# Optimization experiments

Hardware: AMD Instinct MI355X
Metric: run time of the kernel (lower is better)

## Reference

```python
import jax, jax.numpy as jnp
import numpy as np
import math

B, L, HID = 2, 1024, 1536
NH, HD = 24, 64
DSSM = NH * HD            # 1536 (expand = 1)
QKV = 3 * DSSM
DCONV = 2
EPS = 1e-6


def _silu(u):
    return u * jax.nn.sigmoid(u)


def setup_inputs() -> dict:
    key = jax.random.key(0)
    ks = jax.random.split(key, 10)
    x = jax.random.normal(ks[0], (B, L, HID), dtype=jnp.float32)
    w_qkv = jax.random.normal(ks[1], (QKV, HID), dtype=jnp.float32) / math.sqrt(HID)
    conv_w = jax.random.normal(ks[2], (QKV, DCONV), dtype=jnp.float32) * 0.5  # depthwise causal conv, k=2
    w_dt = jax.random.normal(ks[3], (NH, HID), dtype=jnp.float32) * 0.02
    # dt_bias init exactly as in the torch module
    dt = jnp.exp(jax.random.uniform(ks[4], (NH,)) * (math.log(0.1) - math.log(0.001)) + math.log(0.001))
    dt = jnp.clip(dt, 1e-4, None)
    dt_bias = dt + jnp.log(-jnp.expm1(-dt))
    a_log = jnp.log(jax.random.uniform(ks[5], (NH,), minval=1.0, maxval=16.0))
    D = jnp.ones((NH, HD), dtype=jnp.float32)
    w_z = jax.random.normal(ks[6], (DSSM, HID), dtype=jnp.float32) / math.sqrt(HID)
    b_z = jnp.zeros((DSSM,), dtype=jnp.float32)
    rms_w = jnp.ones((DSSM,), dtype=jnp.float32)
    w_o = jax.random.normal(ks[7], (HID, DSSM), dtype=jnp.float32) / math.sqrt(DSSM)
    return dict(x=x, w_qkv=w_qkv, conv_w=conv_w, w_dt=w_dt, dt_bias=dt_bias,
                a_log=a_log, D=D, w_z=w_z, b_z=b_z, rms_w=rms_w, w_o=w_o)


def reference(x, w_qkv, conv_w, w_dt, dt_bias, a_log, D, w_z, b_z, rms_w, w_o):
    # qkv projection  [B,L,3*DSSM]
    qkv = jnp.einsum('blh,qh->blq', x, w_qkv)
    # depthwise causal conv1d (kernel size 2, padding k-1, trimmed to L)
    prev = jnp.pad(qkv, ((0, 0), (1, 0), (0, 0)))[:, :L]
    qkv = _silu(prev * conv_w[:, 0] + qkv * conv_w[:, 1])
    q, k, v = jnp.split(qkv, 3, axis=-1)
    q = q.reshape(B, L, NH, HD)
    k = k.reshape(B, L, NH, HD)
    v = v.reshape(B, L, NH, HD)
    # dt discretization: softplus(dt_proj(x) + dt_bias)   [B,L,NH]
    dt = jax.nn.softplus(jnp.einsum('blh,nh->bln', x, w_dt) + dt_bias)
    A = -jnp.exp(a_log)              # [NH], negative
    dA = dt * A                      # [B,L,NH]
    cs = jnp.transpose(jnp.cumsum(dA, axis=1), (0, 2, 1))   # [B,NH,L]
    diff = cs[:, :, :, None] - cs[:, :, None, :]            # [B,NH,L,L], <=0 on causal part
    causal = jnp.tril(jnp.ones((L, L), dtype=bool))
    decay = jnp.exp(jnp.where(causal, diff, -jnp.inf))      # segment-sum decay matrix
    # quadratic SSD (attention) form of the selective scan
    scores = jnp.einsum('bihd,bjhd->bhij', q, k) * decay
    scores = scores * jnp.transpose(dt, (0, 2, 1))[:, :, None, :]  # dt_j on keys (B-discretization)
    y = jnp.einsum('bhij,bjhd->bihd', scores, v)
    y = y + v * D                    # D skip connection
    y = y.reshape(B, L, DSSM)
    # z gate + RMSNorm + output projection
    z = jnp.einsum('blh,dh->bld', x, w_z) + b_z
    y = y * _silu(z)
    y = y * jax.lax.rsqrt(jnp.mean(y * y, axis=-1, keepdims=True) + EPS) * rms_w
    return jnp.einsum('bld,hd->blh', y, w_o)
```

## Files before the change

### kernel.cpp

```cpp
#include <hip/hip_runtime.h>
#include <hip/hip_bf16.h>
#include <math.h>

#define B_ 2
#define L_ 1024
#define HID_ 1536
#define NH_ 24
#define HD_ 64
#define DSSM_ 1536
#define QKV_ 4608
#define M_ 2048

typedef __attribute__((ext_vector_type(8))) short short8;
typedef __attribute__((ext_vector_type(4))) short short4e;
typedef __attribute__((ext_vector_type(4))) float floatx4;

__device__ __forceinline__ void gload_lds16(const short* g, short* l)
{
    __builtin_amdgcn_global_load_lds(
        (const __attribute__((address_space(1))) void*)g,
        (__attribute__((address_space(3))) void*)l,
        16, 0, 0);
}

__device__ __forceinline__ float bfs2f(short s)
{
    unsigned u = ((unsigned)(unsigned short)s) << 16;
    float f; __builtin_memcpy(&f, &u, 4); return f;
}
__device__ __forceinline__ short f2bfs(float f)
{
    __hip_bfloat16 h = __float2bfloat16(f);
    short s; __builtin_memcpy(&s, &h, 2); return s;
}

__device__ const int kIt[30] = {0,1,2,3,4,5, 6,6, 7,7, 8,8, 9,9, 10,10, 11,11,
                                12,12,12, 13,13,13, 14,14,14, 15,15,15};
__device__ const int kS[30]  = {0,0,0,0,0,0, 0,1, 0,1, 0,1, 0,1, 0,1, 0,1,
                                0,1,2, 0,1,2, 0,1,2, 0,1,2};

#define CN0 (M_ * HID_)
#define CN1 (QKV_ * HID_)
#define CN2 (DSSM_ * HID_)
#define CN3 (HID_ * DSSM_)
__global__ void cast_all_kernel(
    const float* __restrict__ x,  const float* __restrict__ wq,
    const float* __restrict__ wz, const float* __restrict__ wo,
    __hip_bfloat16* __restrict__ xb,
    __hip_bfloat16* __restrict__ wcat,
    __hip_bfloat16* __restrict__ wob)
{
    int i = (blockIdx.x * 256 + threadIdx.x) * 4;
    const float* src; __hip_bfloat16* dst; int off;
    if (i < CN0)                   { src = x;  dst = xb;         off = i; }
    else if (i < CN0 + CN1)        { src = wq; dst = wcat;       off = i - CN0; }
    else if (i < CN0 + CN1 + CN2)  { src = wz; dst = wcat + CN1; off = i - CN0 - CN1; }
    else                           { src = wo; dst = wob;        off = i - CN0 - CN1 - CN2; }
    float4 f = *reinterpret_cast<const float4*>(src + off);
    dst[off]     = __float2bfloat16(f.x);
    dst[off + 1] = __float2bfloat16(f.y);
    dst[off + 2] = __float2bfloat16(f.z);
    dst[off + 3] = __float2bfloat16(f.w);
}

#define MFMA_ __builtin_amdgcn_mfma_f32_16x16x32_bf16
#define BAR_() __builtin_amdgcn_s_barrier()
#define SCHED_ __builtin_amdgcn_sched_barrier(0)

#define CSTR 200

__global__ __launch_bounds__(256, 2) void gemm_qkvz_128(
    const __hip_bfloat16* __restrict__ A,
    const __hip_bfloat16* __restrict__ Bm,
    __hip_bfloat16* __restrict__ qkv_out,
    float* __restrict__ z_out,
    const float* __restrict__ b_z)
{
    extern __shared__ short lds[];
    const int K  = HID_;
    const int NT = K / 64;
    const int tid   = threadIdx.x;
    const int lane  = tid & 63;
    const int wave  = tid >> 6;
    const int col16 = lane & 15;
    const int quad  = lane >> 4;
    const int wm = wave >> 1;
    const int wn = wave & 1;
    const int rowblk = blockIdx.y * 128;
    const int colblk = blockIdx.x * 192;

    const short* Ap = reinterpret_cast<const short*>(A);
    const short* Bp = reinterpret_cast<const short*>(Bm);

    const int o  = tid * 16;
    const int s  = o ^ (((o >> 7) & 7) << 4);
    const int sr = s >> 7;
    const int sc = (s & 127) >> 1;

    const int mask = (col16 & 7) << 4;
    const int e0 = ((quad * 16)      ^ mask) >> 1;
    const int e1 = ((64 + quad * 16) ^ mask) >> 1;
    const int arow = (wm * 64 + col16) * 64;
    const int brow = (wn * 96 + col16) * 64;

    floatx4 acc[4][6] = {};

    auto STAGE_ALL = [&](int c, int t) {
        const short* ga = Ap + (size_t)(rowblk + sr) * K + t * 64 + sc;
        short* da = &lds[c * 8192 + tid * 8];
#pragma unroll
        for (int u = 0; u < 4; ++u)
            gload_lds16(ga + (size_t)(u * 32) * K, da + u * 2048);
        const short* gb = Bp + (size_t)(colblk + sr) * K + t * 64 + sc;
        short* db = &lds[16384 + c * 12288 + tid * 8];
#pragma unroll
        for (int u = 0; u < 6; ++u)
            gload_lds16(gb + (size_t)(u * 32) * K, db + u * 2048);
    };

    STAGE_ALL(0, 0);
    asm volatile("s_waitcnt vmcnt(0)" ::: "memory");
    SCHED_;
    BAR_();

    for (int t = 0; t < NT; ++t) {
        const int cur = t & 1;
        if (t + 1 < NT) STAGE_ALL(cur ^ 1, t + 1);

        const int Ab = cur * 8192;
        const int Bb = 16384 + cur * 12288;
        short8 af0[4], af1[4], bf0[6], bf1[6];
#pragma unroll
        for (int m = 0; m < 4; ++m) {
            af0[m] = *reinterpret_cast<const short8*>(&lds[Ab + arow + m * 1024 + e0]);
            af1[m] = *reinterpret_cast<const short8*>(&lds[Ab + arow + m * 1024 + e1]);
        }
#pragma unroll
        for (int n = 0; n < 6; ++n) {
            bf0[n] = *reinterpret_cast<const short8*>(&lds[Bb + brow + n * 1024 + e0]);
            bf1[n] = *reinterpret_cast<const short8*>(&lds[Bb + brow + n * 1024 + e1]);
        }
        asm volatile("s_waitcnt lgkmcnt(0)" ::: "memory");
        SCHED_;

        __builtin_amdgcn_s_setprio(1);
#pragma unroll
        for (int m = 0; m < 4; ++m)
#pragma unroll
            for (int n = 0; n < 6; ++n) {
                acc[m][n] = MFMA_(af0[m], bf0[n], acc[m][n], 0, 0, 0);
                acc[m][n] = MFMA_(af1[m], bf1[n], acc[m][n], 0, 0, 0);
            }
        __builtin_amdgcn_s_setprio(0);

        asm volatile("s_waitcnt vmcnt(0)" ::: "memory");
        SCHED_;
        BAR_();
    }

    if (blockIdx.x < 24) {
        const int rb = wm * 64 + quad * 4;
        const int cb = wn * 96 + col16;
#pragma unroll
        for (int m = 0; m < 4; ++m)
#pragma unroll
            for (int n = 0; n < 6; ++n)
#pragma unroll
                for (int r = 0; r < 4; ++r)
                    lds[(rb + m * 16 + r) * CSTR + cb + n * 16] =
                        f2bfs(acc[m][n][r]);
        __syncthreads();
        const int row = tid >> 1;
        const int seg = tid & 1;
        const short* srcp = &lds[row * CSTR + seg * 96];
        short* dstp = reinterpret_cast<short*>(qkv_out)
                    + (size_t)(rowblk + row) * QKV_ + colblk + seg * 96;
#pragma unroll
        for (int j = 0; j < 12; ++j)
            *reinterpret_cast<short8*>(dstp + j * 8) =
                *reinterpret_cast<const short8*>(srcp + j * 8);
    } else {
        const int row0  = rowblk + wm * 64;
        const int col0g = colblk + wn * 96 - QKV_;
#pragma unroll
        for (int m = 0; m < 4; ++m)
#pragma unroll
            for (int n = 0; n < 6; ++n)
#pragma unroll
                for (int r = 0; r < 4; ++r) {
                    int row = row0 + m * 16 + quad * 4 + r;
                    int col = col0g + n * 16 + col16;
                    z_out[(size_t)row * DSSM_ + col] = acc[m][n][r] + b_z[col];
                }
    }
}

template<int OUTMODE>
__global__ __launch_bounds__(256) void gemm_nt(
    const __hip_bfloat16* __restrict__ A,
    const __hip_bfloat16* __restrict__ Bm,
    void* __restrict__ Cv,
    const float* __restrict__ bias,
    int M, int N, int K)
{
    const int lane  = threadIdx.x & 63;
    const int wave  = threadIdx.x >> 6;
    const int col16 = lane & 15;
    const int quad  = lane >> 4;
    const int wr    = wave >> 1;
    const int wc    = wave & 1;
    const int rowblk = blockIdx.y * 128;
    const int colblk = blockIdx.x * 128;

    const short* Ap = reinterpret_cast<const short*>(A);
    const short* Bp = reinterpret_cast<const short*>(Bm);

    __shared__ alignas(16) short As[128 * 32];
    __shared__ alignas(16) short Bs[128 * 32];

    const int srow = lane >> 2;
    const int scol = (lane & 3) * 8;

    floatx4 acc[4][4] = {};

    for (int k0 = 0; k0 < K; k0 += 32) {
#pragma unroll
        for (int s2 = 0; s2 < 2; ++s2) {
            const int seg = wave * 2 + s2;
            gload_lds16(Ap + (size_t)(rowblk + seg * 16 + srow) * K + k0 + scol,
                        &As[seg * 512]);
            gload_lds16(Bp + (size_t)(colblk + seg * 16 + srow) * K + k0 + scol,
                        &Bs[seg * 512]);
        }
        __syncthreads();

        short8 af[4], bf[4];
#pragma unroll
        for (int t = 0; t < 4; ++t) {
            af[t] = *reinterpret_cast<const short8*>(
                &As[(wr * 64 + t * 16 + col16) * 32 + quad * 8]);
            bf[t] = *reinterpret_cast<const short8*>(
                &Bs[(wc * 64 + t * 16 + col16) * 32 + quad * 8]);
        }
#pragma unroll
        for (int mt = 0; mt < 4; ++mt)
#pragma unroll
            for (int nt = 0; nt < 4; ++nt)
                acc[mt][nt] = __builtin_amdgcn_mfma_f32_16x16x32_bf16(
                    af[mt], bf[nt], acc[mt][nt], 0, 0, 0);
        __syncthreads();
    }

    const int row0 = rowblk + wr * 64;
    const int col0 = colblk + wc * 64;
#pragma unroll
    for (int mt = 0; mt < 4; ++mt) {
#pragma unroll
        for (int nt = 0; nt < 4; ++nt) {
#pragma unroll
            for (int r = 0; r < 4; ++r) {
                int row = row0 + mt * 16 + quad * 4 + r;
                int col = col0 + nt * 16 + col16;
                float v = acc[mt][nt][r];
                if (OUTMODE == 1) v += bias[col];
                if (OUTMODE == 2)
                    ((__hip_bfloat16*)Cv)[(size_t)row * N + col] = __float2bfloat16(v);
                else
                    ((float*)Cv)[(size_t)row * N + col] = v;
            }
        }
    }
}

__global__ void conv_silu_kernel(
    const __hip_bfloat16* __restrict__ raw,
    const float* __restrict__ conv_w,
    __hip_bfloat16* __restrict__ q,
    __hip_bfloat16* __restrict__ k,
    __hip_bfloat16* __restrict__ v)
{
    int idx8 = blockIdx.x * 256 + threadIdx.x;
    int c8 = (idx8 % (QKV_ / 8)) * 8;
    int ml = idx8 / (QKV_ / 8);
    int l  = ml % L_;
    int b  = ml / L_;

    const short* base = reinterpret_cast<const short*>(raw) + (size_t)ml * QKV_ + c8;
    short8 curv = *reinterpret_cast<const short8*>(base);
    short8 prevv = {};
    if (l > 0) prevv = *reinterpret_cast<const short8*>(base - QKV_);

    float4 w0 = *reinterpret_cast<const float4*>(conv_w + c8 * 2);
    float4 w1 = *reinterpret_cast<const float4*>(conv_w + c8 * 2 + 4);
    float4 w2 = *reinterpret_cast<const float4*>(conv_w + c8 * 2 + 8);
    float4 w3 = *reinterpret_cast<const float4*>(conv_w + c8 * 2 + 12);
    const float wa[16] = {w0.x, w0.y, w0.z, w0.w, w1.x, w1.y, w1.z, w1.w,
                          w2.x, w2.y, w2.z, w2.w, w3.x, w3.y, w3.z, w3.w};

    short8 outv;
#pragma unroll
    for (int j = 0; j < 8; ++j) {
        float u = bfs2f(prevv[j]) * wa[2 * j] + bfs2f(curv[j]) * wa[2 * j + 1];
        u = fmaxf(u, -80.f);
        outv[j] = f2bfs(u / (1.f + __expf(-u)));
    }

    int part = c8 / DSSM_;
    int cc   = c8 % DSSM_;
    int nh   = cc >> 6;
    int d    = cc & 63;
    __hip_bfloat16* dst = (part == 0) ? q : ((part == 1) ? k : v);
    *reinterpret_cast<short8*>(
        reinterpret_cast<short*>(dst) + (((size_t)b * NH_ + nh) * L_ + l) * HD_ + d)
        = outv;
}

__global__ __launch_bounds__(256) void dtproj_kernel(
    const float* __restrict__ x,
    const float* __restrict__ w_dt,
    const float* __restrict__ dt_bias,
    const float* __restrict__ a_log,
    float* __restrict__ dt,
    float* __restrict__ dA)
{
    const int tid  = threadIdx.x;
    const int wave = tid >> 6;
    const int lane = tid & 63;
    const int m0   = blockIdx.x * 8 + wave * 2;

    float4 xa[2][6];
#pragma unroll
    for (int rr = 0; rr < 2; ++rr)
#pragma unroll
        for (int j = 0; j < 6; ++j)
            xa[rr][j] = *reinterpret_cast<const float4*>(
                x + (size_t)(m0 + rr) * HID_ + lane * 4 + j * 256);

    float acc0[NH_], acc1[NH_];
#pragma unroll
    for (int n = 0; n < NH_; ++n) {
        float s0 = 0.f, s1 = 0.f;
#pragma unroll
        for (int j = 0; j < 6; ++j) {
            float4 w = *reinterpret_cast<const float4*>(
                w_dt + (size_t)n * HID_ + lane * 4 + j * 256);
            s0 += xa[0][j].x * w.x + xa[0][j].y * w.y
                + xa[0][j].z * w.z + xa[0][j].w * w.w;
            s1 += xa[1][j].x * w.x + xa[1][j].y * w.y
                + xa[1][j].z * w.z + xa[1][j].w * w.w;
        }
        acc0[n] = s0;
        acc1[n] = s1;
    }

#pragma unroll
    for (int off = 32; off; off >>= 1) {
#pragma unroll
        for (int n = 0; n < NH_; ++n) {
            acc0[n] += __shfl_xor(acc0[n], off, 64);
            acc1[n] += __shfl_xor(acc1[n], off, 64);
        }
    }

    if (lane < NH_) {
        const int n = lane;
        float bias = dt_bias[n];
        float Aval = -__expf(a_log[n]);
        float v0 = acc0[n] + bias;
        float v1 = acc1[n] + bias;
        v0 = (v0 > 20.f) ? v0 : log1pf(__expf(v0));
        v1 = (v1 > 20.f) ? v1 : log1pf(__expf(v1));
        int b0 = m0 / L_, l0 = m0 % L_;
        size_t o0 = ((size_t)b0 * NH_ + n) * L_ + l0;
        dt[o0]     = v0;
        dA[o0]     = v0 * Aval;
        dt[o0 + 1] = v1;
        dA[o0 + 1] = v1 * Aval;
    }
}

__global__ void cumsum_kernel(const float* __restrict__ dA, float* __restrict__ cs)
{
    int bnh  = blockIdx.x;
    int lane = threadIdx.x;
    const float* src = dA + (size_t)bnh * L_;
    float* dst       = cs + (size_t)bnh * L_;

    float loc[16];
    float run = 0.f;
#pragma unroll
    for (int t = 0; t < 16; ++t) { run += src[lane * 16 + t]; loc[t] = run; }
    float tot = run;
    float sc = tot;
#pragma unroll
    for (int off = 1; off < 64; off <<= 1) {
        float o = __shfl_up(sc, off, 64);
        if (lane >= off) sc += o;
    }
    float offset = sc - tot;
#pragma unroll
    for (int t = 0; t < 16; ++t) dst[lane * 16 + t] = loc[t] + offset;
}

__global__ __launch_bounds__(256) void vdt_transpose_kernel(
    const __hip_bfloat16* __restrict__ v,
    const float* __restrict__ dt,
    __hip_bfloat16* __restrict__ vt)
{
    const int lt0 = blockIdx.x * 64;
    const int bnh = blockIdx.z * NH_ + blockIdx.y;
    const int tid = threadIdx.x;

    __shared__ short T[64][72];

    {
        int row = tid >> 2;
        int cc  = (tid & 3) * 16;
        const short* sp = reinterpret_cast<const short*>(v)
                        + ((size_t)bnh * L_ + lt0 + row) * HD_ + cc;
        float dtr = dt[(size_t)bnh * L_ + lt0 + row];
        short8 a = *reinterpret_cast<const short8*>(sp);
        short8 b = *reinterpret_cast<const short8*>(sp + 8);
#pragma unroll
        for (int j = 0; j < 8; ++j) {
            T[row][cc + j]     = f2bfs(bfs2f(a[j]) * dtr);
            T[row][cc + 8 + j] = f2bfs(bfs2f(b[j]) * dtr);
        }
    }
    __syncthreads();
    {
        int d  = tid >> 2;
        int lc = (tid & 3) * 16;
        short8 o0, o1;
#pragma unroll
        for (int j = 0; j < 8; ++j) {
            o0[j] = T[lc + j][d];
            o1[j] = T[lc + 8 + j][d];
        }
        short* dst = reinterpret_cast<short*>(vt)
                   + ((size_t)bnh * HD_ + d) * L_ + lt0 + lc;
        *reinterpret_cast<short8*>(dst)     = o0;
        *reinterpret_cast<short8*>(dst + 8) = o1;
    }
}

__global__ __launch_bounds__(256) void attn_kernel(
    const __hip_bfloat16* __restrict__ q,
    const __hip_bfloat16* __restrict__ k,
    const __hip_bfloat16* __restrict__ vt,
    const float* __restrict__ cs,
    float* __restrict__ p0,
    float* __restrict__ p1,
    float* __restrict__ p2)
{
    const int pidx = blockIdx.x;
    const int it   = kIt[pidx];
    const int sl   = kS[pidx];
    const int nh   = blockIdx.y;
    const int b    = blockIdx.z;
    const int tid  = threadIdx.x;
    const int lane = tid & 63;
    const int wave = tid >> 6;
    const int col  = lane & 15;
    const int quad = lane >> 4;
    const int bnh  = b * NH_ + nh;
    const int iw0  = it * 64 + wave * 16;

    float* pout = (sl == 0) ? p0 : ((sl == 1) ? p1 : p2);

    const short* qp  = reinterpret_cast<const short*>(q);
    const short* kp  = reinterpret_cast<const short*>(k);
    const short* vtp = reinterpret_cast<const short*>(vt);

    __shared__ alignas(16) short Ks[4096];
    __shared__ alignas(16) short Ps[4 * 16 * 72];
    __shared__ float Cj[384];

    const int jbase = sl * 384;
    const int jlim  = min(384, L_ - jbase);
    if (tid < (jlim >> 2))
        *reinterpret_cast<float4*>(&Cj[tid * 4]) =
            *reinterpret_cast<const float4*>(cs + (size_t)bnh * L_ + jbase + tid * 4);

    const short* qrow = qp + ((size_t)bnh * L_ + iw0 + col) * HD_;
    short8 aq0 = *reinterpret_cast<const short8*>(qrow + quad * 8);
    short8 aq1 = *reinterpret_cast<const short8*>(qrow + 32 + quad * 8);

    float csr[4];
#pragma unroll
    for (int r = 0; r < 4; ++r)
        csr[r] = cs[(size_t)bnh * L_ + iw0 + quad * 4 + r];

    auto STAGE_K = [&](int jt2) {
        const short* gk = kp + ((size_t)bnh * L_ + jt2 * 64 + wave * 16 + (lane >> 2)) * HD_
                        + (lane & 3) * 8;
        gload_lds16(gk,      &Ks[wave * 512 + lane * 8]);
        gload_lds16(gk + 32, &Ks[2048 + wave * 512 + lane * 8]);
    };

    const int jt_beg = sl * 6;
    const int jt_end = min(sl * 6 + 5, it);

    STAGE_K(jt_beg);

    floatx4 accO[4] = {};

    for (int jt = jt_beg; jt <= jt_end; ++jt) {
        const int j0 = jt * 64;

        asm volatile("s_waitcnt vmcnt(0)" ::: "memory");
        SCHED_;
        __syncthreads();

        short8 bv[2][4];
#pragma unroll
        for (int c = 0; c < 2; ++c) {
            if (j0 + c * 32 <= iw0 + 15) {
#pragma unroll
                for (int nt = 0; nt < 4; ++nt)
                    bv[c][nt] = *reinterpret_cast<const short8*>(
                        vtp + ((size_t)bnh * HD_ + nt * 16 + col) * L_
                            + j0 + c * 32 + quad * 8);
            }
        }

#pragma unroll
        for (int s = 0; s < 4; ++s) {
            int jsub = j0 + s * 16;
            if (jsub <= iw0 + 15) {
                short8 bk0 = *reinterpret_cast<const short8*>(
                    &Ks[(s * 16 + col) * 32 + quad * 8]);
                short8 bk1 = *reinterpret_cast<const short8*>(
                    &Ks[2048 + (s * 16 + col) * 32 + quad * 8]);
                floatx4 sc = {};
                sc = __builtin_amdgcn_mfma_f32_16x16x32_bf16(aq0, bk0, sc, 0, 0, 0);
                sc = __builtin_amdgcn_mfma_f32_16x16x32_bf16(aq1, bk1, sc, 0, 0, 0);
                int j = jsub + col;
                float csj = Cj[j - jbase];
#pragma unroll
                for (int r = 0; r < 4; ++r) {
                    int i = iw0 + quad * 4 + r;
                    float e = (j <= i) ? __expf(csr[r] - csj) : 0.f;
                    Ps[wave * 1152 + (quad * 4 + r) * 72 + s * 16 + col] =
                        f2bfs(sc[r] * e);
                }
            } else if (j0 + (s >> 1) * 32 <= iw0 + 15) {
#pragma unroll
                for (int r = 0; r < 4; ++r)
                    Ps[wave * 1152 + (quad * 4 + r) * 72 + s * 16 + col] = 0;
            }
        }

#pragma unroll
        for (int c = 0; c < 2; ++c) {
            if (j0 + c * 32 > iw0 + 15) continue;
            short8 pa = *reinterpret_cast<const short8*>(
                &Ps[wave * 1152 + col * 72 + c * 32 + quad * 8]);
#pragma unroll
            for (int nt = 0; nt < 4; ++nt)
                accO[nt] = __builtin_amdgcn_mfma_f32_16x16x32_bf16(
                    pa, bv[c][nt], accO[nt], 0, 0, 0);
        }

        __syncthreads();
        if (jt < jt_end) STAGE_K(jt + 1);
    }

#pragma unroll
    for (int nt = 0; nt < 4; ++nt) {
#pragma unroll
        for (int r = 0; r < 4; ++r) {
            int i  = iw0 + quad * 4 + r;
            int dv = nt * 16 + col;
            pout[((size_t)b * L_ + i) * DSSM_ + nh * HD_ + dv] = accO[nt][r];
        }
    }
}

__global__ __launch_bounds__(256) void gate_rms_kernel(
    const float* __restrict__ p0,
    const float* __restrict__ p1,
    const float* __restrict__ p2,
    const float* __restrict__ z,
    const __hip_bfloat16* __restrict__ v,
    const float* __restrict__ Dm,
    const float* __restrict__ rms_w,
    __hip_bfloat16* __restrict__ yn)
{
    int m   = blockIdx.x;
    int b   = m / L_;
    int l   = m % L_;
    int tid = threadIdx.x;
    size_t base = (size_t)m * DSSM_;
    const bool has1 = (l >= 384);
    const bool has2 = (l >= 768);

    floatx4 acc4[2] = {};
    float ss = 0.f;
#pragma unroll
    for (int t = 0; t < 2; ++t) {
        int i4 = t * 256 + tid;
        if (i4 < DSSM_ / 4) {
            int c  = i4 * 4;
            int nh = c >> 6, d = c & 63;
            floatx4 p = *reinterpret_cast<const floatx4*>(p0 + base + c);
            if (has1) p += *reinterpret_cast<const floatx4*>(p1 + base + c);
            if (has2) p += *reinterpret_cast<const floatx4*>(p2 + base + c);
            floatx4 dm = *reinterpret_cast<const floatx4*>(Dm + c);
            floatx4 zz = *reinterpret_cast<const floatx4*>(z + base + c);
            short4e vv = *reinterpret_cast<const short4e*>(
                reinterpret_cast<const short*>(v)
                + (((size_t)b * NH_ + nh) * L_ + l) * HD_ + d);
            floatx4 g;
#pragma unroll
            for (int j = 0; j < 4; ++j) {
                float yv = p[j] + bfs2f(vv[j]) * dm[j];
                float zv = fmaxf(zz[j], -80.f);
                float gv = yv * (zv / (1.f + __expf(-zv)));
                ss += gv * gv;
                g[j] = gv;
            }
            acc4[t] = g;
        }
    }
#pragma unroll
    for (int off = 32; off; off >>= 1) ss += __shfl_xor(ss, off, 64);
    __shared__ float red[4];
    if ((tid & 63) == 0) red[tid >> 6] = ss;
    __syncthreads();
    ss = red[0] + red[1] + red[2] + red[3];
    float r = rsqrtf(ss / (float)DSSM_ + 1e-6f);
#pragma unroll
    for (int t = 0; t < 2; ++t) {
        int i4 = t * 256 + tid;
        if (i4 < DSSM_ / 4) {
            int c = i4 * 4;
            floatx4 rw = *reinterpret_cast<const floatx4*>(rms_w + c);
            short4e o;
#pragma unroll
            for (int j = 0; j < 4; ++j)
                o[j] = f2bfs(acc4[t][j] * r * rw[j]);
            *reinterpret_cast<short4e*>(
                reinterpret_cast<short*>(yn) + base + c) = o;
        }
    }
}

extern "C" void kernel_launch(void* const* d_in, const int* in_sizes, int n_in,
                              void* d_out, int out_size, void* d_ws, size_t ws_size,
                              hipStream_t stream)
{
    const float* x       = (const float*)d_in[0];
    const float* w_qkv   = (const float*)d_in[1];
    const float* conv_w  = (const float*)d_in[2];
    const float* w_dt    = (const float*)d_in[3];
    const float* dt_bias = (const float*)d_in[4];
    const float* a_log   = (const float*)d_in[5];
    const float* Dm      = (const float*)d_in[6];
    const float* w_z     = (const float*)d_in[7];
    const float* b_z     = (const float*)d_in[8];
    const float* rms_w   = (const float*)d_in[9];
    const float* w_o     = (const float*)d_in[10];
    float* out = (float*)d_out;

    char* ws = (char*)d_ws;

    __hip_bfloat16* xb    = (__hip_bfloat16*)(ws);
    __hip_bfloat16* wob   = (__hip_bfloat16*)(ws + 6291456);
    float*          zbuf  = (float*)(ws + 11010048);
    __hip_bfloat16* wcat  = (__hip_bfloat16*)(ws + 23592960);
    __hip_bfloat16* qkvb  = (__hip_bfloat16*)(ws + 42467328);
    __hip_bfloat16* qb    = (__hip_bfloat16*)(ws + 61341696);
    __hip_bfloat16* kb    = (__hip_bfloat16*)(ws + 67633152);
    __hip_bfloat16* vb    = (__hip_bfloat16*)(ws + 73924608);
    float* dt   = (float*)(ws + 80216064);
    float* dA   = (float*)(ws + 80412672);
    float* cs   = (float*)(ws + 80609280);
    __hip_bfloat16* vtb = (__hip_bfloat16*)(ws);
    __hip_bfloat16* yn  = (__hip_bfloat16*)(ws);
    float* p0 = (float*)(ws + 23592960);
    float* p1 = (float*)(ws + 36175872);
    float* p2 = (float*)(ws + 48758784);

    static bool attr_set = false;
    if (!attr_set) {
        (void)hipFuncSetAttribute(reinterpret_cast<const void*>(gemm_qkvz_128),
                                  hipFuncAttributeMaxDynamicSharedMemorySize,
                                  81920);
        attr_set = true;
    }

    cast_all_kernel<<<(CN0 + CN1 + CN2 + CN3) / 1024, 256, 0, stream>>>(
        x, w_qkv, w_z, w_o, xb, wcat, wob);

    gemm_qkvz_128<<<dim3((QKV_ + DSSM_) / 192, M_ / 128), 256, 81920, stream>>>(
        xb, wcat, qkvb, zbuf, b_z);

    conv_silu_kernel<<<(B_ * L_ * QKV_ / 8) / 256, 256, 0, stream>>>(
        qkvb, conv_w, qb, kb, vb);

    dtproj_kernel<<<M_ / 8, 256, 0, stream>>>(x, w_dt, dt_bias, a_log, dt, dA);

    cumsum_kernel<<<B_ * NH_, 64, 0, stream>>>(dA, cs);

    vdt_transpose_kernel<<<dim3(L_ / 64, NH_, B_), 256, 0, stream>>>(vb, dt, vtb);

    attn_kernel<<<dim3(30, NH_, B_), 256, 0, stream>>>(
        qb, kb, vtb, cs, p0, p1, p2);

    gate_rms_kernel<<<M_, 256, 0, stream>>>(p0, p1, p2, zbuf, vb, Dm, rms_w, yn);

    gemm_nt<0><<<dim3(HID_ / 128, M_ / 128), 256, 0, stream>>>(
        yn, wob, (void*)out, nullptr, M_, HID_, DSSM_);
}
```

Baseline: 276.0 us.

## Fuse x bf16 cast into dtproj and remap attention blocks per XCD

The x-to-bf16 conversion moves out of the combined cast kernel and into dtproj_kernel, which already loads x in fp32, so x is no longer read a second time. dtproj and cumsum now run before the QKV GEMM, since the GEMM needs xb. The attention launch becomes a 1D grid of 1440 blocks, remapped so that every block of one (batch, head) pair lands on the same XCD, which should improve L2 reuse of that pair's K/V. The remap assumes round-robin dispatch of blocks across 8 XCDs.

```diff
diff --git a/kernel.cpp b/kernel.cpp
--- a/kernel.cpp
+++ b/kernel.cpp
@@ -43,19 +43,17 @@
 #define CN1 (QKV_ * HID_)
 #define CN2 (DSSM_ * HID_)
 #define CN3 (HID_ * DSSM_)
-__global__ void cast_all_kernel(
-    const float* __restrict__ x,  const float* __restrict__ wq,
+__global__ void cast_w_kernel(
+    const float* __restrict__ wq,
     const float* __restrict__ wz, const float* __restrict__ wo,
-    __hip_bfloat16* __restrict__ xb,
     __hip_bfloat16* __restrict__ wcat,
     __hip_bfloat16* __restrict__ wob)
 {
     int i = (blockIdx.x * 256 + threadIdx.x) * 4;
     const float* src; __hip_bfloat16* dst; int off;
-    if (i < CN0)                   { src = x;  dst = xb;         off = i; }
-    else if (i < CN0 + CN1)        { src = wq; dst = wcat;       off = i - CN0; }
-    else if (i < CN0 + CN1 + CN2)  { src = wz; dst = wcat + CN1; off = i - CN0 - CN1; }
-    else                           { src = wo; dst = wob;        off = i - CN0 - CN1 - CN2; }
+    if (i < CN1)             { src = wq; dst = wcat;       off = i; }
+    else if (i < CN1 + CN2)  { src = wz; dst = wcat + CN1; off = i - CN1; }
+    else                     { src = wo; dst = wob;        off = i - CN1 - CN2; }
     float4 f = *reinterpret_cast<const float4*>(src + off);
     dst[off]     = __float2bfloat16(f.x);
     dst[off + 1] = __float2bfloat16(f.y);
@@ -321,7 +319,8 @@
     const float* __restrict__ dt_bias,
     const float* __restrict__ a_log,
     float* __restrict__ dt,
-    float* __restrict__ dA)
+    float* __restrict__ dA,
+    __hip_bfloat16* __restrict__ xb)
 {
     const int tid  = threadIdx.x;
     const int wave = tid >> 6;
@@ -335,6 +334,18 @@
         for (int j = 0; j < 6; ++j)
             xa[rr][j] = *reinterpret_cast<const float4*>(
                 x + (size_t)(m0 + rr) * HID_ + lane * 4 + j * 256);
+
+    short* xbp = reinterpret_cast<short*>(xb);
+#pragma unroll
+    for (int rr = 0; rr < 2; ++rr)
+#pragma unroll
+        for (int j = 0; j < 6; ++j) {
+            short4e ov;
+            ov[0] = f2bfs(xa[rr][j].x); ov[1] = f2bfs(xa[rr][j].y);
+            ov[2] = f2bfs(xa[rr][j].z); ov[3] = f2bfs(xa[rr][j].w);
+            *reinterpret_cast<short4e*>(
+                xbp + (size_t)(m0 + rr) * HID_ + lane * 4 + j * 256) = ov;
+        }
 
     float acc0[NH_], acc1[NH_];
 #pragma unroll
@@ -453,11 +464,15 @@
     float* __restrict__ p1,
     float* __restrict__ p2)
 {
-    const int pidx = blockIdx.x;
+    const int bid  = blockIdx.x;
+    const int xcd  = bid & 7;
+    const int tq   = bid >> 3;
+    const int g    = (tq / 30) * 8 + xcd;
+    const int pidx = tq % 30;
     const int it   = kIt[pidx];
     const int sl   = kS[pidx];
-    const int nh   = blockIdx.y;
-    const int b    = blockIdx.z;
+    const int b    = g / NH_;
+    const int nh   = g % NH_;
     const int tid  = threadIdx.x;
     const int lane = tid & 63;
     const int wave = tid >> 6;
@@ -690,8 +705,13 @@
         attr_set = true;
     }
 
-    cast_all_kernel<<<(CN0 + CN1 + CN2 + CN3) / 1024, 256, 0, stream>>>(
-        x, w_qkv, w_z, w_o, xb, wcat, wob);
+    cast_w_kernel<<<(CN1 + CN2 + CN3) / 1024, 256, 0, stream>>>(
+        w_qkv, w_z, w_o, wcat, wob);
+
+    dtproj_kernel<<<M_ / 8, 256, 0, stream>>>(
+        x, w_dt, dt_bias, a_log, dt, dA, xb);
+
+    cumsum_kernel<<<B_ * NH_, 64, 0, stream>>>(dA, cs);
 
     gemm_qkvz_128<<<dim3((QKV_ + DSSM_) / 192, M_ / 128), 256, 81920, stream>>>(
         xb, wcat, qkvb, zbuf, b_z);
@@ -699,13 +719,9 @@
     conv_silu_kernel<<<(B_ * L_ * QKV_ / 8) / 256, 256, 0, stream>>>(
         qkvb, conv_w, qb, kb, vb);
 
-    dtproj_kernel<<<M_ / 8, 256, 0, stream>>>(x, w_dt, dt_bias, a_log, dt, dA);
-
-    cumsum_kernel<<<B_ * NH_, 64, 0, stream>>>(dA, cs);
-
     vdt_transpose_kernel<<<dim3(L_ / 64, NH_, B_), 256, 0, stream>>>(vb, dt, vtb);
 
-    attn_kernel<<<dim3(30, NH_, B_), 256, 0, stream>>>(
+    attn_kernel<<<1440, 256, 0, stream>>>(
         qb, kb, vtb, cs, p0, p1, p2);
 
     gate_rms_kernel<<<M_, 256, 0, stream>>>(p0, p1, p2, zbuf, vb, Dm, rms_w, yn);
```

Measured after the change: 273.4 us. No clear change (-0.9%).
